# Kernel tuning notes

Measured on AMD Instinct MI355X. Metric: run time of the kernel, lower is better.

## Reference

```python
import jax, jax.numpy as jnp
import numpy as np

# Dimensions
O, D, F_LSOA = 128, 128, 64      # origins, destinations, LSOA feature dim
T, FE, H = 128, 16, 64           # max seq len, edge_feature_dim, gru_hidden
NH, NO, PH = 128, 64, 128        # node_hidden, node_out, pair_hidden
P = O * D                        # number of O-D pairs


def _mlp3(x, W1, b1, W2, b2, W3, b3):
    # Linear->ReLU->Linear->ReLU->Linear (dropout is identity in eval mode)
    h = jax.nn.relu(x @ W1 + b1)
    h = jax.nn.relu(h @ W2 + b2)
    return h @ W3 + b3


def setup_inputs() -> dict:
    key = jax.random.key(0)
    ks = jax.random.split(key, 32)

    def rn(k, shape, s):
        return jax.random.normal(k, shape, dtype=jnp.float32) * s

    inp = {
        "O_feats": rn(ks[0], (O, F_LSOA), 1.0),
        "D_feats": rn(ks[1], (D, F_LSOA), 1.0),
        "seqs": rn(ks[2], (P, T, FE), 1.0),
        "lengths": jax.random.randint(ks[3], (P,), 1, T + 1, dtype=jnp.int32),
        # enc_O
        "WO1": rn(ks[4], (F_LSOA, NH), 0.05), "bO1": jnp.zeros((NH,), jnp.float32),
        "WO2": rn(ks[5], (NH, NH), 0.05),     "bO2": jnp.zeros((NH,), jnp.float32),
        "WO3": rn(ks[6], (NH, NO), 0.05),     "bO3": jnp.zeros((NO,), jnp.float32),
        # enc_D
        "WD1": rn(ks[7], (F_LSOA, NH), 0.05), "bD1": jnp.zeros((NH,), jnp.float32),
        "WD2": rn(ks[8], (NH, NH), 0.05),     "bD2": jnp.zeros((NH,), jnp.float32),
        "WD3": rn(ks[9], (NH, NO), 0.05),     "bD3": jnp.zeros((NO,), jnp.float32),
        # pair_head: 2*node_out -> pair_hidden -> 1
        "Wp1": rn(ks[10], (2 * NO, PH), 0.05), "bp1": jnp.zeros((PH,), jnp.float32),
        "Wp2": rn(ks[11], (PH, 1), 0.05),      "bp2": jnp.zeros((1,), jnp.float32),
        # GRU (gate order r, z, n as in PyTorch)
        "W_ih": rn(ks[12], (FE, 3 * H), 0.1),  "b_ih": jnp.zeros((3 * H,), jnp.float32),
        "W_hh": rn(ks[13], (H, 3 * H), 0.1),   "b_hh": jnp.zeros((3 * H,), jnp.float32),
        # seq_head
        "Ws": rn(ks[14], (H, 1), 0.1),         "bs": jnp.zeros((1,), jnp.float32),
    }
    return inp


def reference(O_feats, D_feats, seqs, lengths,
              WO1, bO1, WO2, bO2, WO3, bO3,
              WD1, bD1, WD2, bD2, WD3, bD3,
              Wp1, bp1, Wp2, bp2,
              W_ih, W_hh, b_ih, b_hh,
              Ws, bs):
    # Node encoders
    eo = _mlp3(O_feats, WO1, bO1, WO2, bO2, WO3, bO3)   # [O, NO]
    ed = _mlp3(D_feats, WD1, bD1, WD2, bD2, WD3, bD3)   # [D, NO]

    # Pairwise score: concat(eo, ed) -> MLP -> softplus
    pair_in = jnp.concatenate([
        jnp.broadcast_to(eo[:, None, :], (O, D, NO)),
        jnp.broadcast_to(ed[None, :, :], (O, D, NO)),
    ], axis=-1)                                          # [O, D, 2*NO]
    hp = jax.nn.relu(pair_in @ Wp1 + bp1)                # [O, D, PH]
    z_pair = (hp @ Wp2 + bp2)[..., 0]                    # [O, D]
    s_pair = jax.nn.softplus(z_pair)

    # Length-masked GRU over all O*D padded sequences (equiv. to pack_padded)
    xT = jnp.swapaxes(seqs, 0, 1)                        # [T, P, FE]
    h0 = jnp.zeros((P, H), jnp.float32)

    def step(h, inp):
        xt, t = inp
        gx = xt @ W_ih + b_ih                            # [P, 3H]
        gh = h @ W_hh + b_hh                             # [P, 3H]
        xr, xz, xn = jnp.split(gx, 3, axis=-1)
        hr, hz, hn = jnp.split(gh, 3, axis=-1)
        r = jax.nn.sigmoid(xr + hr)
        zg = jax.nn.sigmoid(xz + hz)
        n = jnp.tanh(xn + r * hn)
        h_new = (1.0 - zg) * n + zg * h
        h = jnp.where((t < lengths)[:, None], h_new, h)  # freeze past seq end
        return h, None

    h_last, _ = jax.lax.scan(step, h0, (xT, jnp.arange(T)))  # [P, H]

    p_seq = jax.nn.sigmoid(h_last @ Ws + bs)[:, 0].reshape(O, D)
    return jnp.sum(s_pair * p_seq)
```

## Files before the change

### kernel.cpp

```cpp
#include <hip/hip_runtime.h>
#include <hip/hip_bf16.h>

#define O_N 128
#define D_N 128
#define F_LS 64
#define T_MAX 128
#define FE_N 16
#define H_GRU 64
#define NH 128
#define NO 64
#define PH 128

typedef _Float16 f16;
typedef __fp16 hf2 __attribute__((ext_vector_type(2)));
typedef f16 f16x4 __attribute__((ext_vector_type(4)));
typedef f16 f16x8 __attribute__((ext_vector_type(8)));
typedef float f32x4 __attribute__((ext_vector_type(4)));

__device__ __forceinline__ float fast_sigmoid(float x) {
    return __builtin_amdgcn_rcpf(1.f + __expf(-x));
}

__global__ __launch_bounds__(128) void k_enc(
    const float* __restrict__ O_feats, const float* __restrict__ D_feats,
    const float* __restrict__ WO1, const float* __restrict__ bO1,
    const float* __restrict__ WO2, const float* __restrict__ bO2,
    const float* __restrict__ WO3, const float* __restrict__ bO3,
    const float* __restrict__ WD1, const float* __restrict__ bD1,
    const float* __restrict__ WD2, const float* __restrict__ bD2,
    const float* __restrict__ WD3, const float* __restrict__ bD3,
    const float* __restrict__ Wp1, const float* __restrict__ bp1,
    float* __restrict__ PA, float* __restrict__ PBt, float* __restrict__ d_out)
{
    __shared__ float h1[NH];
    __shared__ float h2[NH];
    __shared__ float ev[NO];
    const int b = blockIdx.x;
    const int enc = b >> 7;
    const int row = b & 127;
    const int t = threadIdx.x;
    if (b == 0 && t == 0) d_out[0] = 0.f;

    const float* x  = (enc ? D_feats : O_feats) + row * F_LS;
    const float* W1 = enc ? WD1 : WO1;  const float* b1 = enc ? bD1 : bO1;
    const float* W2 = enc ? WD2 : WO2;  const float* b2 = enc ? bD2 : bO2;
    const float* W3 = enc ? WD3 : WO3;  const float* b3 = enc ? bD3 : bO3;

    float a = b1[t];
    #pragma unroll 8
    for (int k = 0; k < F_LS; ++k) a += x[k] * W1[k * NH + t];
    h1[t] = fmaxf(a, 0.f);
    __syncthreads();

    a = b2[t];
    #pragma unroll 8
    for (int k = 0; k < NH; ++k) a += h1[k] * W2[k * NH + t];
    h2[t] = fmaxf(a, 0.f);
    __syncthreads();

    if (t < NO) {
        a = b3[t];
        #pragma unroll 8
        for (int k = 0; k < NH; ++k) a += h2[k] * W3[k * NO + t];
        ev[t] = a;
    }
    __syncthreads();

    const float* Wp = Wp1 + (enc ? NO * PH : 0);
    a = 0.f;
    #pragma unroll 8
    for (int k = 0; k < NO; ++k) a += ev[k] * Wp[k * PH + t];
    if (enc) PBt[t * 128 + row] = a + bp1[t];
    else     PA[row * PH + t] = a;
}

__global__ __launch_bounds__(128) void k_pair(
    const float* __restrict__ PA, const float* __restrict__ PBt,
    const float* __restrict__ Wp2, const float* __restrict__ bp2,
    float* __restrict__ s_pair)
{
    const int i = blockIdx.x;
    const int j = threadIdx.x;
    __shared__ float pa[PH];
    __shared__ float w2s[PH];
    pa[j]  = PA[i * PH + j];
    w2s[j] = Wp2[j];
    __syncthreads();
    float acc = 0.f;
    #pragma unroll 8
    for (int c = 0; c < PH; ++c)
        acc += w2s[c] * fmaxf(pa[c] + PBt[c * 128 + j], 0.f);
    float z = acc + bp2[0];
    float sp = fmaxf(z, 0.f) + log1pf(__expf(-fabsf(z)));
    s_pair[i * 128 + j] = sp;
}

__global__ __launch_bounds__(1024) void k_sort(
    const int* __restrict__ lengths, int* __restrict__ perm)
{
    __shared__ int cnt[130];
    __shared__ int suf[130];
    const int t = threadIdx.x;
    if (t < 130) cnt[t] = 0;
    __syncthreads();
    for (int i = t; i < 16384; i += 1024) atomicAdd(&cnt[lengths[i]], 1);
    __syncthreads();
    if (t < 130) suf[t] = cnt[t];
    __syncthreads();
    for (int d = 1; d < 130; d <<= 1) {
        int v = 0;
        if (t < 130) { v = suf[t]; if (t + d < 130) v += suf[t + d]; }
        __syncthreads();
        if (t < 130) suf[t] = v;
        __syncthreads();
    }
    if (t < 129) cnt[t] = (t + 1 < 130) ? suf[t + 1] : 0;
    __syncthreads();
    for (int i = t; i < 16384; i += 1024) {
        int pos = atomicAdd(&cnt[lengths[i]], 1);
        perm[pos] = i;
    }
}

__global__ __launch_bounds__(256, 4) void k_gru(
    const float* __restrict__ seqs, const int* __restrict__ lengths,
    const int* __restrict__ perm,
    const float* __restrict__ W_ih, const float* __restrict__ b_ih,
    const float* __restrict__ W_hh, const float* __restrict__ b_hh,
    const float* __restrict__ Ws, const float* __restrict__ bs,
    const float* __restrict__ s_pair, float* __restrict__ d_out)
{
    __shared__ __align__(16) f16 hbuf[2][16 * 72];
    __shared__ __align__(16) float xbuf[2][8][16][16];
    __shared__ float red[64];
    const int tid = threadIdx.x;
    const int w  = tid >> 6;
    const int l  = tid & 63;
    const int q  = l >> 4;
    const int n  = l & 15;
    const int c  = w * 16 + n;
    const int colbase = w * 16 + q * 4;
    const int pb = blockIdx.x * 16;
    const float S_RZ = -1.4426950408889634f;
    const float S_N  =  2.8853900817779268f;

    f16x8 wh[3][2], wi[3];
    #pragma unroll
    for (int gg = 0; gg < 3; ++gg) {
        const int gb = gg * 64;
        const float s = (gg < 2) ? S_RZ : S_N;
        #pragma unroll
        for (int ks = 0; ks < 2; ++ks)
            #pragma unroll
            for (int j = 0; j < 8; ++j)
                wh[gg][ks][j] = (f16)(W_hh[(ks * 32 + q * 8 + j) * 192 + gb + c] * s);
        #pragma unroll
        for (int j = 0; j < 8; ++j) {
            int k = q * 8 + j;
            wi[gg][j] = (k < FE_N) ? (f16)(W_ih[k * 192 + gb + c] * s) : (f16)0.f;
        }
    }
    f32x4 c_r, c_z, c_hn, c_xn;
    float wsc[4];
    #pragma unroll
    for (int r = 0; r < 4; ++r) {
        int col = colbase + r;
        c_r[r]  = S_RZ * (b_ih[col] + b_hh[col]);
        c_z[r]  = S_RZ * (b_ih[64 + col] + b_hh[64 + col]);
        c_hn[r] = S_N * b_hh[128 + col];
        c_xn[r] = S_N * b_ih[128 + col];
        wsc[r]  = Ws[col];
    }
    const int myp   = perm[pb + n];
    const int mylen = lengths[myp];
    int ml = mylen;
    ml = max(ml, __shfl_xor(ml, 1));
    ml = max(ml, __shfl_xor(ml, 2));
    ml = max(ml, __shfl_xor(ml, 4));
    ml = max(ml, __shfl_xor(ml, 8));
    const int maxlen = __builtin_amdgcn_readfirstlane(ml);

    const float* xsrc = seqs + (size_t)perm[pb + (l >> 2)] * (T_MAX * FE_N)
                       + (l & 3) * 4;

    if (tid < 144) { f16x8 z8 = {}; *(f16x8*)&hbuf[0][tid * 8] = z8; }

    #pragma unroll
    for (int rr = 0; rr < 2; ++rr) {
        const int r8 = w + rr * 4;
        __builtin_amdgcn_global_load_lds(
            (const __attribute__((address_space(1))) void*)(xsrc + (size_t)r8 * FE_N),
            (__attribute__((address_space(3))) void*)&xbuf[0][r8][0][0], 16, 0, 0);
    }
    float hold[4] = {0.f, 0.f, 0.f, 0.f};
    const f16x8 zero8 = {};
    __syncthreads();

    #pragma unroll 1
    for (int t = 0; t < maxlen; ++t) {
        const int cur = t & 1;
        const int xb  = (t >> 3) & 1;
        const int row = t & 7;
        const f16* hb  = hbuf[cur];
        f16*       hbw = hbuf[cur ^ 1];
        f16x8 bh0 = *(const f16x8*)&hb[n * 72 + 8 * q];
        f16x8 bh1 = *(const f16x8*)&hb[n * 72 + 32 + 8 * q];

        if (row == 0 && t + 8 < maxlen) {
            const int nb = xb ^ 1;
            #pragma unroll
            for (int rr = 0; rr < 2; ++rr) {
                const int rl = w + rr * 4;
                int rg = t + 8 + rl;
                rg = rg < T_MAX ? rg : T_MAX - 1;
                __builtin_amdgcn_global_load_lds(
                    (const __attribute__((address_space(1))) void*)(xsrc + (size_t)rg * FE_N),
                    (__attribute__((address_space(3))) void*)&xbuf[nb][rl][0][0], 16, 0, 0);
            }
        }

        f16x8 ax = zero8;
        if (q < 2) {
            const float* xr = &xbuf[xb][row][n][q * 8];
            float4 a0 = *(const float4*)xr;
            float4 a1 = *(const float4*)(xr + 4);
            union { f16x8 v8; hf2 v2[4]; } u;
            u.v2[0] = __builtin_amdgcn_cvt_pkrtz(a0.x, a0.y);
            u.v2[1] = __builtin_amdgcn_cvt_pkrtz(a0.z, a0.w);
            u.v2[2] = __builtin_amdgcn_cvt_pkrtz(a1.x, a1.y);
            u.v2[3] = __builtin_amdgcn_cvt_pkrtz(a1.z, a1.w);
            ax = u.v8;
        }

        f32x4 ar = __builtin_amdgcn_mfma_f32_16x16x32_f16(wi[0], ax, c_r, 0, 0, 0);
        f32x4 az = __builtin_amdgcn_mfma_f32_16x16x32_f16(wi[1], ax, c_z, 0, 0, 0);
        f32x4 xn = __builtin_amdgcn_mfma_f32_16x16x32_f16(wi[2], ax, c_xn, 0, 0, 0);
        ar = __builtin_amdgcn_mfma_f32_16x16x32_f16(wh[0][0], bh0, ar, 0, 0, 0);
        ar = __builtin_amdgcn_mfma_f32_16x16x32_f16(wh[0][1], bh1, ar, 0, 0, 0);
        az = __builtin_amdgcn_mfma_f32_16x16x32_f16(wh[1][0], bh0, az, 0, 0, 0);
        az = __builtin_amdgcn_mfma_f32_16x16x32_f16(wh[1][1], bh1, az, 0, 0, 0);
        f32x4 hn = __builtin_amdgcn_mfma_f32_16x16x32_f16(wh[2][0], bh0, c_hn, 0, 0, 0);
        hn = __builtin_amdgcn_mfma_f32_16x16x32_f16(wh[2][1], bh1, hn, 0, 0, 0);

        const bool live = (t < mylen);
        #pragma unroll
        for (int r = 0; r < 4; ++r) {
            float rg    = __builtin_amdgcn_rcpf(1.f + __builtin_amdgcn_exp2f(ar[r]));
            float zg    = __builtin_amdgcn_rcpf(1.f + __builtin_amdgcn_exp2f(az[r]));
            float inner = fmaf(rg, hn[r], xn[r]);
            float nn    = fmaf(-2.f, __builtin_amdgcn_rcpf(1.f + __builtin_amdgcn_exp2f(inner)), 1.f);
            float hnew  = fmaf(zg, hold[r] - nn, nn);
            hold[r] = live ? hnew : hold[r];
        }
        union { f16x4 v4; hf2 v2[2]; } hu;
        hu.v2[0] = __builtin_amdgcn_cvt_pkrtz(hold[0], hold[1]);
        hu.v2[1] = __builtin_amdgcn_cvt_pkrtz(hold[2], hold[3]);
        *(f16x4*)&hbw[n * 72 + colbase] = hu.v4;
        __syncthreads();
    }

    float part = hold[0] * wsc[0] + hold[1] * wsc[1] +
                 hold[2] * wsc[2] + hold[3] * wsc[3];
    part += __shfl_xor(part, 16);
    part += __shfl_xor(part, 32);
    if (l < 16) red[w * 16 + n] = part;
    __syncthreads();
    if (tid < 16) {
        float s = red[tid] + red[16 + tid] + red[32 + tid] + red[48 + tid];
        float pv = fast_sigmoid(s + bs[0]);
        float contrib = s_pair[perm[pb + tid]] * pv;
        #pragma unroll
        for (int off = 1; off < 16; off <<= 1)
            contrib += __shfl_xor(contrib, off);
        if (tid == 0) atomicAdd(d_out, contrib);
    }
}

extern "C" void kernel_launch(void* const* d_in, const int* in_sizes, int n_in,
                              void* d_out, int out_size, void* d_ws, size_t ws_size,
                              hipStream_t stream)
{
    const float* O_feats = (const float*)d_in[0];
    const float* D_feats = (const float*)d_in[1];
    const float* seqs    = (const float*)d_in[2];
    const int*   lengths = (const int*)d_in[3];
    const float* WO1 = (const float*)d_in[4];  const float* bO1 = (const float*)d_in[5];
    const float* WO2 = (const float*)d_in[6];  const float* bO2 = (const float*)d_in[7];
    const float* WO3 = (const float*)d_in[8];  const float* bO3 = (const float*)d_in[9];
    const float* WD1 = (const float*)d_in[10]; const float* bD1 = (const float*)d_in[11];
    const float* WD2 = (const float*)d_in[12]; const float* bD2 = (const float*)d_in[13];
    const float* WD3 = (const float*)d_in[14]; const float* bD3 = (const float*)d_in[15];
    const float* Wp1 = (const float*)d_in[16]; const float* bp1 = (const float*)d_in[17];
    const float* Wp2 = (const float*)d_in[18]; const float* bp2 = (const float*)d_in[19];
    const float* W_ih = (const float*)d_in[20]; const float* b_ih = (const float*)d_in[21];
    const float* W_hh = (const float*)d_in[22]; const float* b_hh = (const float*)d_in[23];
    const float* Ws   = (const float*)d_in[24]; const float* bs   = (const float*)d_in[25];

    float* out    = (float*)d_out;
    float* PA     = (float*)d_ws;
    float* PBt    = PA + 128 * 128;
    float* s_pair = PBt + 128 * 128;
    int*   perm   = (int*)(s_pair + 16384);

    k_enc<<<256, 128, 0, stream>>>(O_feats, D_feats,
                                   WO1, bO1, WO2, bO2, WO3, bO3,
                                   WD1, bD1, WD2, bD2, WD3, bD3,
                                   Wp1, bp1, PA, PBt, out);
    k_pair<<<128, 128, 0, stream>>>(PA, PBt, Wp2, bp2, s_pair);
    k_sort<<<1, 1024, 0, stream>>>(lengths, perm);
    k_gru<<<1024, 256, 0, stream>>>(seqs, lengths, perm, W_ih, b_ih, W_hh, b_hh,
                                    Ws, bs, s_pair, out);
}
```

Baseline: 328.7 us.

## Merge sort into encoder kernel, fold pair head into GRU, stagger x prefetch

The counting sort now runs as an extra block of the encoder kernel, and the pair-head MLP plus softplus is computed inside the GRU epilogue. This cuts the launch count from four to two and removes the s_pair round trip. The x staging buffer is relaid as float4 slots so the LDS reads are conflict-free, and each block starts its prefetch at a different row offset so blocks do not all issue global loads in the same step. The per-step __syncthreads is replaced by explicit waitcnt plus s_barrier, waiting on vector memory only once every 8 steps; this adds some redundant pair-head work per block and relies on getting the manual wait placement right.

Measured after the change: 327.3 us. Within noise of the previous version (-0.4%).

```diff
diff --git a/kernel.cpp b/kernel.cpp
--- a/kernel.cpp
+++ b/kernel.cpp
@@ -21,7 +21,7 @@
     return __builtin_amdgcn_rcpf(1.f + __expf(-x));
 }
 
-__global__ __launch_bounds__(128) void k_enc(
+__global__ __launch_bounds__(256) void k_pre(
     const float* __restrict__ O_feats, const float* __restrict__ D_feats,
     const float* __restrict__ WO1, const float* __restrict__ bO1,
     const float* __restrict__ WO2, const float* __restrict__ bO2,
@@ -30,15 +30,42 @@
     const float* __restrict__ WD2, const float* __restrict__ bD2,
     const float* __restrict__ WD3, const float* __restrict__ bD3,
     const float* __restrict__ Wp1, const float* __restrict__ bp1,
-    float* __restrict__ PA, float* __restrict__ PBt, float* __restrict__ d_out)
+    const int* __restrict__ lengths,
+    float* __restrict__ PA, float* __restrict__ PBt,
+    int* __restrict__ perm, float* __restrict__ d_out)
 {
+    const int t = threadIdx.x;
+    if (blockIdx.x == 256) {
+        __shared__ int cnt[130];
+        __shared__ int suf[130];
+        if (t < 130) cnt[t] = 0;
+        __syncthreads();
+        for (int i = t; i < 16384; i += 256) atomicAdd(&cnt[lengths[i]], 1);
+        __syncthreads();
+        if (t < 130) suf[t] = cnt[t];
+        __syncthreads();
+        for (int d = 1; d < 130; d <<= 1) {
+            int v = 0;
+            if (t < 130) { v = suf[t]; if (t + d < 130) v += suf[t + d]; }
+            __syncthreads();
+            if (t < 130) suf[t] = v;
+            __syncthreads();
+        }
+        if (t < 129) cnt[t] = (t + 1 < 130) ? suf[t + 1] : 0;
+        __syncthreads();
+        for (int i = t; i < 16384; i += 256) {
+            int pos = atomicAdd(&cnt[lengths[i]], 1);
+            perm[pos] = i;
+        }
+        return;
+    }
+
     __shared__ float h1[NH];
     __shared__ float h2[NH];
     __shared__ float ev[NO];
     const int b = blockIdx.x;
     const int enc = b >> 7;
     const int row = b & 127;
-    const int t = threadIdx.x;
     if (b == 0 && t == 0) d_out[0] = 0.f;
 
     const float* x  = (enc ? D_feats : O_feats) + row * F_LS;
@@ -46,79 +73,37 @@
     const float* W2 = enc ? WD2 : WO2;  const float* b2 = enc ? bD2 : bO2;
     const float* W3 = enc ? WD3 : WO3;  const float* b3 = enc ? bD3 : bO3;
 
-    float a = b1[t];
-    #pragma unroll 8
-    for (int k = 0; k < F_LS; ++k) a += x[k] * W1[k * NH + t];
-    h1[t] = fmaxf(a, 0.f);
-    __syncthreads();
-
-    a = b2[t];
-    #pragma unroll 8
-    for (int k = 0; k < NH; ++k) a += h1[k] * W2[k * NH + t];
-    h2[t] = fmaxf(a, 0.f);
+    if (t < 128) {
+        float a = b1[t];
+        #pragma unroll 8
+        for (int k = 0; k < F_LS; ++k) a += x[k] * W1[k * NH + t];
+        h1[t] = fmaxf(a, 0.f);
+    }
+    __syncthreads();
+
+    if (t < 128) {
+        float a = b2[t];
+        #pragma unroll 8
+        for (int k = 0; k < NH; ++k) a += h1[k] * W2[k * NH + t];
+        h2[t] = fmaxf(a, 0.f);
+    }
     __syncthreads();
 
     if (t < NO) {
-        a = b3[t];
+        float a = b3[t];
         #pragma unroll 8
         for (int k = 0; k < NH; ++k) a += h2[k] * W3[k * NO + t];
         ev[t] = a;
     }
     __syncthreads();
 
-    const float* Wp = Wp1 + (enc ? NO * PH : 0);
-    a = 0.f;
-    #pragma unroll 8
-    for (int k = 0; k < NO; ++k) a += ev[k] * Wp[k * PH + t];
-    if (enc) PBt[t * 128 + row] = a + bp1[t];
-    else     PA[row * PH + t] = a;
-}
-
-__global__ __launch_bounds__(128) void k_pair(
-    const float* __restrict__ PA, const float* __restrict__ PBt,
-    const float* __restrict__ Wp2, const float* __restrict__ bp2,
-    float* __restrict__ s_pair)
-{
-    const int i = blockIdx.x;
-    const int j = threadIdx.x;
-    __shared__ float pa[PH];
-    __shared__ float w2s[PH];
-    pa[j]  = PA[i * PH + j];
-    w2s[j] = Wp2[j];
-    __syncthreads();
-    float acc = 0.f;
-    #pragma unroll 8
-    for (int c = 0; c < PH; ++c)
-        acc += w2s[c] * fmaxf(pa[c] + PBt[c * 128 + j], 0.f);
-    float z = acc + bp2[0];
-    float sp = fmaxf(z, 0.f) + log1pf(__expf(-fabsf(z)));
-    s_pair[i * 128 + j] = sp;
-}
-
-__global__ __launch_bounds__(1024) void k_sort(
-    const int* __restrict__ lengths, int* __restrict__ perm)
-{
-    __shared__ int cnt[130];
-    __shared__ int suf[130];
-    const int t = threadIdx.x;
-    if (t < 130) cnt[t] = 0;
-    __syncthreads();
-    for (int i = t; i < 16384; i += 1024) atomicAdd(&cnt[lengths[i]], 1);
-    __syncthreads();
-    if (t < 130) suf[t] = cnt[t];
-    __syncthreads();
-    for (int d = 1; d < 130; d <<= 1) {
-        int v = 0;
-        if (t < 130) { v = suf[t]; if (t + d < 130) v += suf[t + d]; }
-        __syncthreads();
-        if (t < 130) suf[t] = v;
-        __syncthreads();
-    }
-    if (t < 129) cnt[t] = (t + 1 < 130) ? suf[t + 1] : 0;
-    __syncthreads();
-    for (int i = t; i < 16384; i += 1024) {
-        int pos = atomicAdd(&cnt[lengths[i]], 1);
-        perm[pos] = i;
+    if (t < 128) {
+        const float* Wp = Wp1 + (enc ? NO * PH : 0);
+        float a = 0.f;
+        #pragma unroll 8
+        for (int k = 0; k < NO; ++k) a += ev[k] * Wp[k * PH + t];
+        if (enc) PBt[t * 128 + row] = a + bp1[t];
+        else     PA[row * PH + t] = a;
     }
 }
 
@@ -128,10 +113,12 @@
     const float* __restrict__ W_ih, const float* __restrict__ b_ih,
     const float* __restrict__ W_hh, const float* __restrict__ b_hh,
     const float* __restrict__ Ws, const float* __restrict__ bs,
-    const float* __restrict__ s_pair, float* __restrict__ d_out)
+    const float* __restrict__ PA, const float* __restrict__ PBt,
+    const float* __restrict__ Wp2, const float* __restrict__ bp2,
+    float* __restrict__ d_out)
 {
     __shared__ __align__(16) f16 hbuf[2][16 * 72];
-    __shared__ __align__(16) float xbuf[2][8][16][16];
+    __shared__ __align__(16) float4 xbuf[2][8][64];
     __shared__ float red[64];
     const int tid = threadIdx.x;
     const int w  = tid >> 6;
@@ -141,6 +128,7 @@
     const int c  = w * 16 + n;
     const int colbase = w * 16 + q * 4;
     const int pb = blockIdx.x * 16;
+    const int srow = blockIdx.x & 3;
     const float S_RZ = -1.4426950408889634f;
     const float S_N  =  2.8853900817779268f;
 
@@ -180,8 +168,8 @@
     ml = max(ml, __shfl_xor(ml, 8));
     const int maxlen = __builtin_amdgcn_readfirstlane(ml);
 
-    const float* xsrc = seqs + (size_t)perm[pb + (l >> 2)] * (T_MAX * FE_N)
-                       + (l & 3) * 4;
+    const float* xsrc = seqs + (size_t)perm[pb + (l & 15)] * (T_MAX * FE_N)
+                       + (l >> 4) * 4;
 
     if (tid < 144) { f16x8 z8 = {}; *(f16x8*)&hbuf[0][tid * 8] = z8; }
 
@@ -190,7 +178,7 @@
         const int r8 = w + rr * 4;
         __builtin_amdgcn_global_load_lds(
             (const __attribute__((address_space(1))) void*)(xsrc + (size_t)r8 * FE_N),
-            (__attribute__((address_space(3))) void*)&xbuf[0][r8][0][0], 16, 0, 0);
+            (__attribute__((address_space(3))) void*)&xbuf[0][r8][0], 16, 0, 0);
     }
     float hold[4] = {0.f, 0.f, 0.f, 0.f};
     const f16x8 zero8 = {};
@@ -206,24 +194,24 @@
         f16x8 bh0 = *(const f16x8*)&hb[n * 72 + 8 * q];
         f16x8 bh1 = *(const f16x8*)&hb[n * 72 + 32 + 8 * q];
 
-        if (row == 0 && t + 8 < maxlen) {
+        if (row == srow && (t - srow) + 8 < maxlen) {
             const int nb = xb ^ 1;
+            const int tp8 = (t - srow) + 8;
             #pragma unroll
             for (int rr = 0; rr < 2; ++rr) {
                 const int rl = w + rr * 4;
-                int rg = t + 8 + rl;
+                int rg = tp8 + rl;
                 rg = rg < T_MAX ? rg : T_MAX - 1;
                 __builtin_amdgcn_global_load_lds(
                     (const __attribute__((address_space(1))) void*)(xsrc + (size_t)rg * FE_N),
-                    (__attribute__((address_space(3))) void*)&xbuf[nb][rl][0][0], 16, 0, 0);
+                    (__attribute__((address_space(3))) void*)&xbuf[nb][rl][0], 16, 0, 0);
             }
         }
 
         f16x8 ax = zero8;
         if (q < 2) {
-            const float* xr = &xbuf[xb][row][n][q * 8];
-            float4 a0 = *(const float4*)xr;
-            float4 a1 = *(const float4*)(xr + 4);
+            float4 a0 = xbuf[xb][row][32 * q + n];
+            float4 a1 = xbuf[xb][row][32 * q + 16 + n];
             union { f16x8 v8; hf2 v2[4]; } u;
             u.v2[0] = __builtin_amdgcn_cvt_pkrtz(a0.x, a0.y);
             u.v2[1] = __builtin_amdgcn_cvt_pkrtz(a0.z, a0.w);
@@ -256,7 +244,10 @@
         hu.v2[0] = __builtin_amdgcn_cvt_pkrtz(hold[0], hold[1]);
         hu.v2[1] = __builtin_amdgcn_cvt_pkrtz(hold[2], hold[3]);
         *(f16x4*)&hbw[n * 72 + colbase] = hu.v4;
-        __syncthreads();
+
+        if (row == 7) asm volatile("s_waitcnt vmcnt(0)" ::: "memory");
+        asm volatile("s_waitcnt lgkmcnt(0)" ::: "memory");
+        __builtin_amdgcn_s_barrier();
     }
 
     float part = hold[0] * wsc[0] + hold[1] * wsc[1] +
@@ -265,14 +256,36 @@
     part += __shfl_xor(part, 32);
     if (l < 16) red[w * 16 + n] = part;
     __syncthreads();
-    if (tid < 16) {
-        float s = red[tid] + red[16 + tid] + red[32 + tid] + red[48 + tid];
+
+    const int pp = tid >> 4;
+    const int u  = tid & 15;
+    const int pidx = perm[pb + pp];
+    const int ii = pidx >> 7;
+    const int jj = pidx & 127;
+    float acc = 0.f;
+    #pragma unroll
+    for (int cc = u; cc < PH; cc += 16)
+        acc += Wp2[cc] * fmaxf(PA[ii * PH + cc] + PBt[cc * 128 + jj], 0.f);
+    acc += __shfl_xor(acc, 1);
+    acc += __shfl_xor(acc, 2);
+    acc += __shfl_xor(acc, 4);
+    acc += __shfl_xor(acc, 8);
+    float contrib = 0.f;
+    if (u == 0) {
+        float z  = acc + bp2[0];
+        float sp = fmaxf(z, 0.f) + log1pf(__expf(-fabsf(z)));
+        float s  = red[pp] + red[16 + pp] + red[32 + pp] + red[48 + pp];
         float pv = fast_sigmoid(s + bs[0]);
-        float contrib = s_pair[perm[pb + tid]] * pv;
+        contrib  = sp * pv;
+    }
+    __syncthreads();
+    if (u == 0) red[pp] = contrib;
+    __syncthreads();
+    if (tid == 0) {
+        float tot = 0.f;
         #pragma unroll
-        for (int off = 1; off < 16; off <<= 1)
-            contrib += __shfl_xor(contrib, off);
-        if (tid == 0) atomicAdd(d_out, contrib);
+        for (int k = 0; k < 16; ++k) tot += red[k];
+        atomicAdd(d_out, tot);
     }
 }
 
@@ -299,15 +312,12 @@
     float* out    = (float*)d_out;
     float* PA     = (float*)d_ws;
     float* PBt    = PA + 128 * 128;
-    float* s_pair = PBt + 128 * 128;
-    int*   perm   = (int*)(s_pair + 16384);
-
-    k_enc<<<256, 128, 0, stream>>>(O_feats, D_feats,
+    int*   perm   = (int*)(PBt + 128 * 128);
+
+    k_pre<<<257, 256, 0, stream>>>(O_feats, D_feats,
                                    WO1, bO1, WO2, bO2, WO3, bO3,
                                    WD1, bD1, WD2, bD2, WD3, bD3,
-                                   Wp1, bp1, PA, PBt, out);
-    k_pair<<<128, 128, 0, stream>>>(PA, PBt, Wp2, bp2, s_pair);
-    k_sort<<<1, 1024, 0, stream>>>(lengths, perm);
+                                   Wp1, bp1, lengths, PA, PBt, perm, out);
     k_gru<<<1024, 256, 0, stream>>>(seqs, lengths, perm, W_ih, b_ih, W_hh, b_hh,
-                                    Ws, bs, s_pair, out);
+                                    Ws, bs, PA, PBt, Wp2, bp2, out);
 }
```
